# Optimization experiments

Measured on AMD Instinct MI355X. Metric: run time of the kernel, lower is better.

Reference implementation:

```python
import jax, jax.numpy as jnp
import numpy as np

GAMMA = 0.3          # surrogate gradient scale (LinearSpikeMC.gamma)
K = 2                # num_channels: multi-compartment count
T = 3                # timesteps
B = 4                # batch
LABELS = 10
CONV_CFG = [64, 64, 128, 128, 256, 256, 256, 512, 512, 512, 512, 512, 512]
POOL_AFTER = {1, 3, 6, 9}  # avg-pool after these conv indices (VGG16 'A' positions)


@jax.custom_vjp
def spike_mc(even, odd):
    # one-hot multi-compartment spike: fire where even>0 AND odd>=0
    return jnp.where((even > 0.0) & (odd >= 0.0), 1.0, 0.0).astype(even.dtype)

def _spike_fwd(even, odd):
    return spike_mc(even, odd), (even, odd)

def _spike_bwd(res, g):
    even, odd = res
    ge = GAMMA * jnp.maximum(1.0 - jnp.abs(even), 0.0) * g
    go = -GAMMA * jnp.maximum(1.0 - jnp.abs(odd), 0.0) * g
    # torch backward loop never writes the last odd compartment's grad
    go = go.at[-1].set(0.0)
    return ge, go

spike_mc.defvjp(_spike_fwd, _spike_bwd)


def conv3x3(x, w):
    return jax.lax.conv_general_dilated(
        x, w, (1, 1), 'SAME', dimension_numbers=('NCHW', 'OIHW', 'NCHW'))


def avgpool2(x):
    b, c, h, w = x.shape
    return x.reshape(b, c, h // 2, 2, w // 2, 2).mean(axis=(3, 5))


def lif(mem, syn, thr, leak):
    # leaky integrate; compartment i fires when 2^i*thr < mem <= 2^{i+1}*thr
    mem = leak * mem + syn
    pw = (2.0 ** jnp.arange(K, dtype=mem.dtype)).reshape((K,) + (1,) * mem.ndim)
    even = mem[None] / (pw * thr) - 1.0
    odd = 1.0 - mem[None] / (2.0 * pw * thr)
    sp = spike_mc(even, odd)            # [K, ...] one-hot spikes
    val = jnp.sum(pw * sp, axis=0)      # decoded value sum_i 2^i * s_i
    mem = mem - thr * val               # soft reset (reset_to_zero=0)
    return mem, val


def setup_inputs():
    key = jax.random.key(0)
    ks = jax.random.split(key, 32)
    inp = {"x": jax.random.normal(ks[0], (B, 3, 32, 32), jnp.float32)}
    in_c = 3
    for i, out_c in enumerate(CONV_CFG):
        std = float(np.sqrt(2.0 / (9.0 * out_c)))  # kaiming init from _initialize_weights2
        inp[f"w{i}"] = jax.random.normal(ks[1 + i], (out_c, in_c, 3, 3), jnp.float32) * std
        in_c = out_c
    inp["fc0"] = jax.random.normal(ks[20], (4096, 512 * 2 * 2), jnp.float32) * 0.01
    inp["fc1"] = jax.random.normal(ks[21], (4096, 4096), jnp.float32) * 0.01
    inp["fc2"] = jax.random.normal(ks[22], (LABELS, 4096), jnp.float32) * 0.01
    inp["thr"] = jnp.ones((15,), jnp.float32)   # per-layer thresholds
    inp["leak"] = jnp.ones((15,), jnp.float32)  # per-layer leaks
    return inp


def reference(x, w0, w1, w2, w3, w4, w5, w6, w7, w8, w9, w10, w11, w12,
              fc0, fc1, fc2, thr, leak):
    conv_ws = [w0, w1, w2, w3, w4, w5, w6, w7, w8, w9, w10, w11, w12]
    b = x.shape[0]
    # membranes sized at each conv's output resolution (neuron_init)
    mems = []
    s = 32
    for i, c in enumerate(CONV_CFG):
        mems.append(jnp.zeros((b, c, s, s), x.dtype))
        if i in POOL_AFTER:
            s //= 2
    carry0 = (tuple(mems),
              jnp.zeros((b, 4096), x.dtype),
              jnp.zeros((b, 4096), x.dtype),
              jnp.zeros((b, fc2.shape[0]), x.dtype))

    def step(carry, _):
        mems_c, m0, m1, logits = carry
        out = x  # analog input each timestep (input_encoding=1)
        new = []
        for i in range(13):
            m, out = lif(mems_c[i], conv3x3(out, conv_ws[i]), thr[i], leak[i])
            new.append(m)
            if i in POOL_AFTER:
                out = avgpool2(out)
        out = out.reshape(b, -1)
        m0, out = lif(m0, out @ fc0.T, thr[13], leak[13])
        m1, out = lif(m1, out @ fc1.T, thr[14], leak[14])
        logits = logits + out @ fc2.T  # final linear accumulates, no spiking
        return (tuple(new), m0, m1, logits), None

    carry, _ = jax.lax.scan(step, carry0, None, length=T)
    return carry[3]
```

## Files before the change

kernel.cpp:

```cpp
#include <hip/hip_runtime.h>


#define BATCH 4

__device__ __forceinline__ float lif_update(float mem_in, float syn, float thr,
                                            float leak, float* mem_out) {
    float m = leak * mem_in + syn;
    float val = 0.f;
    if ((m / thr - 1.f > 0.f) && (1.f - m / (2.f * thr) >= 0.f)) val += 1.f;
    if ((m / (2.f * thr) - 1.f > 0.f) && (1.f - m / (4.f * thr) >= 0.f)) val += 2.f;
    *mem_out = m - thr * val;
    return val;
}

__global__ void conv_lif0_kernel(const float* __restrict__ in,
                                 const float* __restrict__ w,
                                 float* __restrict__ out0,
                                 float* __restrict__ out1,
                                 float* __restrict__ out2,
                                 const float* __restrict__ thr_v,
                                 const float* __restrict__ leak_v,
                                 int IC, int OC, int H, int W, int n) {
    int idx = blockIdx.x * blockDim.x + threadIdx.x;
    if (idx >= n) return;
    int x  = idx % W;
    int y  = (idx / W) % H;
    int oc = (idx / (W * H)) % OC;
    int b  = idx / (W * H * OC);

    const float* wp = w + (size_t)oc * IC * 9;
    const float* ip = in + (size_t)b * IC * H * W;

    float syn = 0.f;
    for (int ic = 0; ic < IC; ++ic) {
        const float* ipc = ip + (size_t)ic * H * W;
        const float* wpc = wp + ic * 9;
#pragma unroll
        for (int ky = 0; ky < 3; ++ky) {
            int yy = y + ky - 1;
            if (yy < 0 || yy >= H) continue;
#pragma unroll
            for (int kx = 0; kx < 3; ++kx) {
                int xx = x + kx - 1;
                if (xx < 0 || xx >= W) continue;
                syn = fmaf(ipc[yy * W + xx], wpc[ky * 3 + kx], syn);
            }
        }
    }
    float thr = thr_v[0], leak = leak_v[0];
    float m = 0.f;
    float v0 = lif_update(m, syn, thr, leak, &m);
    float v1 = lif_update(m, syn, thr, leak, &m);
    float v2 = lif_update(m, syn, thr, leak, &m);
    out0[idx] = v0;
    out1[idx] = v1;
    out2[idx] = v2;
}

template <int NW, int W_>
__device__ __forceinline__ void stage_tiles(float* __restrict__ dst, int tid,
                                            int rnd, int icpw, int y0,
                                            const float* __restrict__ i0,
                                            const float* __restrict__ i1,
                                            const float* __restrict__ i2) {
    constexpr int TWD = W_ + 2;
    constexpr int TH = 64 / W_ + 2;
    constexpr int TILE = TH * TWD;
    constexpr int HW = W_ * W_;
    constexpr int TOT = NW * 3 * TILE;
    for (int s = tid; s < TOT; s += NW * 64) {
        int icg = s / (3 * TILE);
        int rem = s - icg * 3 * TILE;
        int t = rem / TILE;
        int p = rem - t * TILE;
        int r = p / TWD;
        int c = p - r * TWD;
        int ic = icg * icpw + rnd;
        int gy = y0 + r - 1;
        int gx = c - 1;
        const float* pt = (t == 0) ? i0 : ((t == 1) ? i1 : i2);
        float val = 0.f;
        if (gy >= 0 && gy < W_ && gx >= 0 && gx < W_)
            val = pt[(size_t)ic * HW + gy * W_ + gx];
        dst[s] = val;
    }
}

template <int OCT, int NW, int POOL, int W_>
__global__ __launch_bounds__(NW * 64)
void conv_mid3_kernel(const float* __restrict__ in0,
                      const float* __restrict__ in1,
                      const float* __restrict__ in2,
                      const float* __restrict__ w,
                      float* __restrict__ out0,
                      float* __restrict__ out1,
                      float* __restrict__ out2,
                      const float* __restrict__ thr_v,
                      const float* __restrict__ leak_v,
                      int layer, int IC, int OC) {
    constexpr int HW = W_ * W_;
    constexpr int RPW = 64 / W_;
    constexpr int TH = RPW + 2;
    constexpr int TWD = W_ + 2;
    constexpr int TILE = TH * TWD;
    constexpr int CHUNKS = HW / 64;

    int tid = threadIdx.x;
    int lane = tid & 63;
    int wv = tid >> 6;
    int ocg = OC / OCT;
    int bid = blockIdx.x;
    int g  = bid % ocg;
    int ch = (bid / ocg) % CHUNKS;
    int b  = bid / (ocg * CHUNKS);
    int y0 = ch * RPW;
    int oc0 = g * OCT;

    size_t boff = (size_t)b * IC * HW;
    const float* i0 = in0 + boff;
    const float* i1 = in1 + boff;
    const float* i2 = in2 + boff;
    float* const outs[3] = {out0, out1, out2};
    const float* wbase = w + (size_t)oc0 * IC * 9;

    int icpw = IC / NW;

    __shared__ float stage[2][NW * 3 * TILE];

    float acc[3][OCT];
#pragma unroll
    for (int t = 0; t < 3; ++t)
#pragma unroll
        for (int q = 0; q < OCT; ++q) acc[t][q] = 0.f;

    int r0 = lane / W_;
    int c0 = lane % W_;

    stage_tiles<NW, W_>(stage[0], tid, 0, icpw, y0, i0, i1, i2);
    __syncthreads();

    for (int rnd = 0; rnd < icpw; ++rnd) {
        int buf = rnd & 1;
        if (rnd + 1 < icpw)
            stage_tiles<NW, W_>(stage[buf ^ 1], tid, rnd + 1, icpw, y0, i0, i1, i2);

        int ic = wv * icpw + rnd;
        const float* wp = wbase + (size_t)ic * 9;
        float wvv[OCT][9];
#pragma unroll
        for (int q = 0; q < OCT; ++q) {
            const float* wq = wp + (size_t)q * IC * 9;
#pragma unroll
            for (int k = 0; k < 9; ++k) wvv[q][k] = wq[k];
        }

        const float* sb = stage[buf] + wv * (3 * TILE);
#pragma unroll
        for (int t = 0; t < 3; ++t) {
            const float* tp = sb + t * TILE + r0 * TWD + c0;
            float tv[9];
#pragma unroll
            for (int ky = 0; ky < 3; ++ky)
#pragma unroll
                for (int kx = 0; kx < 3; ++kx)
                    tv[ky * 3 + kx] = tp[ky * TWD + kx];
#pragma unroll
            for (int q = 0; q < OCT; ++q)
#pragma unroll
                for (int k = 0; k < 9; ++k)
                    acc[t][q] = fmaf(tv[k], wvv[q][k], acc[t][q]);
        }
        __syncthreads();
    }

    __shared__ float red[NW][OCT][64];
    __shared__ float vals[OCT][64];
    float thr = thr_v[layer], leak = leak_v[layer];
    float mem_reg = 0.f;
    int eq = tid >> 6, ep = tid & 63;
    constexpr int Wo = W_ / 2, Ho = W_ / 2;

#pragma unroll
    for (int t = 0; t < 3; ++t) {
        __syncthreads();
#pragma unroll
        for (int q = 0; q < OCT; ++q) red[wv][q][lane] = acc[t][q];
        __syncthreads();
        if (tid < OCT * 64) {
            float sum = 0.f;
#pragma unroll
            for (int q = 0; q < NW; ++q) sum += red[q][eq][ep];
            float val = lif_update(mem_reg, sum, thr, leak, &mem_reg);
            if (POOL) {
                vals[eq][ep] = val;
            } else {
                size_t idx = (size_t)(b * OC + oc0 + eq) * HW + ch * 64 + ep;
                outs[t][idx] = val;
            }
        }
        if (POOL) {
            __syncthreads();
            if (tid < OCT * 16) {
                int q = tid >> 4, s = tid & 15;
                int pr = s / Wo, pc = s % Wo;
                float pv = 0.25f * (vals[q][(2 * pr) * W_ + 2 * pc] +
                                    vals[q][(2 * pr) * W_ + 2 * pc + 1] +
                                    vals[q][(2 * pr + 1) * W_ + 2 * pc] +
                                    vals[q][(2 * pr + 1) * W_ + 2 * pc + 1]);
                size_t pidx = ((size_t)(b * OC + oc0 + q) * Ho +
                               (ch * (RPW >> 1) + pr)) * Wo + pc;
                outs[t][pidx] = pv;
            }
        }
    }
}

template <int S, int NW, int POOL>
__global__ __launch_bounds__(NW * 64)
void conv_small4_3_kernel(const float* __restrict__ in0,
                          const float* __restrict__ in1,
                          const float* __restrict__ in2,
                          const float* __restrict__ w,
                          float* __restrict__ out0,
                          float* __restrict__ out1,
                          float* __restrict__ out2,
                          const float* __restrict__ thr_v,
                          const float* __restrict__ leak_v,
                          int layer, int IC, int OC) {
    constexpr int SS = S * S;
    constexpr int M = 4 * SS;
    constexpr int LOG2M = (S == 4) ? 6 : 4;
    int tid = threadIdx.x;
    int lane = tid & 63;
    int wv = tid >> 6;
    int oc = blockIdx.x;

    const float* const ins[3] = {in0, in1, in2};
    float* const outs[3] = {out0, out1, out2};
    const float* wrow = w + (size_t)oc * IC * 9;

    __shared__ float red[NW][M];
    __shared__ float pvs[M];
    float thr = thr_v[layer], leak = leak_v[layer];
    float mem_reg = 0.f;

#pragma unroll
    for (int t = 0; t < 3; ++t) {
        const float* inb = ins[t];
        float acc[M];
#pragma unroll
        for (int i = 0; i < M; ++i) acc[i] = 0.f;

        for (int ic = lane + (wv << 6); ic < IC; ic += NW * 64) {
            const float* wp = wrow + (size_t)ic * 9;
            float wvv[9];
#pragma unroll
            for (int k = 0; k < 9; ++k) wvv[k] = wp[k];
#pragma unroll
            for (int b = 0; b < 4; ++b) {
                const float4* ip = (const float4*)(inb + (size_t)(b * IC + ic) * SS);
                float pv[SS];
#pragma unroll
                for (int q = 0; q < SS / 4; ++q) {
                    float4 t4 = ip[q];
                    pv[4 * q + 0] = t4.x;
                    pv[4 * q + 1] = t4.y;
                    pv[4 * q + 2] = t4.z;
                    pv[4 * q + 3] = t4.w;
                }
#pragma unroll
                for (int y = 0; y < S; ++y)
#pragma unroll
                    for (int x = 0; x < S; ++x) {
                        float a = acc[b * SS + y * S + x];
#pragma unroll
                        for (int ky = 0; ky < 3; ++ky) {
                            int yy = y + ky - 1;
                            if (yy < 0 || yy >= S) continue;
#pragma unroll
                            for (int kx = 0; kx < 3; ++kx) {
                                int xx = x + kx - 1;
                                if (xx < 0 || xx >= S) continue;
                                a = fmaf(pv[yy * S + xx], wvv[ky * 3 + kx], a);
                            }
                        }
                        acc[b * SS + y * S + x] = a;
                    }
            }
        }

#pragma unroll
        for (int step = 0; step < LOG2M; ++step) {
            const int offx = 1 << step;
            const int half = M >> (step + 1);
            const bool hi = (lane & offx) != 0;
#pragma unroll
            for (int i = 0; i < half; ++i) {
                float sent = hi ? acc[i] : acc[i + half];
                float got = __shfl_xor(sent, offx);
                acc[i] = (hi ? acc[i + half] : acc[i]) + got;
            }
        }
        float sum = acc[0];
#pragma unroll
        for (int offx = M; offx < 64; offx <<= 1) sum += __shfl_xor(sum, offx);

        __syncthreads();
        int o = (int)(__brev((unsigned)(lane & (M - 1))) >> (32 - LOG2M));
        if (lane < M) red[wv][o] = sum;
        __syncthreads();

        if (tid < M) {
            float tot = 0.f;
#pragma unroll
            for (int q = 0; q < NW; ++q) tot += red[q][tid];
            int b = tid / SS, p = tid % SS;
            float val = lif_update(mem_reg, tot, thr, leak, &mem_reg);
            if (POOL) {
                pvs[tid] = val;
            } else {
                size_t idx = (size_t)(b * OC + oc) * SS + p;
                outs[t][idx] = val;
            }
        }
        if (POOL) {
            __syncthreads();
            constexpr int Sh = S / 2, SSh = Sh * Sh;
            if (tid < 4 * SSh) {
                int b = tid / SSh, q = tid % SSh;
                int pr = q / Sh, pc = q % Sh;
                float pv = 0.25f * (pvs[b * SS + (2 * pr) * S + 2 * pc] +
                                    pvs[b * SS + (2 * pr) * S + 2 * pc + 1] +
                                    pvs[b * SS + (2 * pr + 1) * S + 2 * pc] +
                                    pvs[b * SS + (2 * pr + 1) * S + 2 * pc + 1]);
                outs[t][((size_t)(b * OC + oc) * Sh + pr) * Sh + pc] = pv;
            }
        }
    }
}

__global__ void fc_lif3_kernel(const float* __restrict__ in0,
                               const float* __restrict__ in1,
                               const float* __restrict__ in2,
                               const float* __restrict__ w,
                               float* __restrict__ out0,
                               float* __restrict__ out1,
                               float* __restrict__ out2,
                               const float* __restrict__ thr_v,
                               const float* __restrict__ leak_v,
                               int layer, int Kd, int N) {
    int wave = (blockIdx.x * blockDim.x + threadIdx.x) >> 6;
    int lane = threadIdx.x & 63;
    if (wave >= N) return;
    int j = wave;
    int K4 = Kd >> 2;
    const float4* wp = (const float4*)(w + (size_t)j * Kd);
    const float4* ip[3] = {(const float4*)in0, (const float4*)in1, (const float4*)in2};
    float* const outs[3] = {out0, out1, out2};

    float a[3][4];
#pragma unroll
    for (int t = 0; t < 3; ++t)
#pragma unroll
        for (int b = 0; b < 4; ++b) a[t][b] = 0.f;

    for (int k = lane; k < K4; k += 64) {
        float4 wv = wp[k];
#pragma unroll
        for (int t = 0; t < 3; ++t)
#pragma unroll
            for (int b = 0; b < 4; ++b) {
                float4 v = ip[t][b * K4 + k];
                a[t][b] = fmaf(wv.x, v.x, fmaf(wv.y, v.y,
                          fmaf(wv.z, v.z, fmaf(wv.w, v.w, a[t][b]))));
            }
    }
#pragma unroll
    for (int t = 0; t < 3; ++t)
#pragma unroll
        for (int b = 0; b < 4; ++b)
#pragma unroll
            for (int off = 32; off > 0; off >>= 1)
                a[t][b] += __shfl_xor(a[t][b], off);

    if (lane == 0) {
        float thr = thr_v[layer], leak = leak_v[layer];
#pragma unroll
        for (int b = 0; b < BATCH; ++b) {
            float m = 0.f;
#pragma unroll
            for (int t = 0; t < 3; ++t) {
                float val = lif_update(m, a[t][b], thr, leak, &m);
                outs[t][(size_t)b * N + j] = val;
            }
        }
    }
}

__global__ void fc2_acc3_kernel(const float* __restrict__ in0,
                                const float* __restrict__ in1,
                                const float* __restrict__ in2,
                                const float* __restrict__ w,
                                float* __restrict__ logits,
                                int Kd, int L) {
    int o = blockIdx.x;
    int l = o % L;
    int b = o / L;
    int K4 = Kd >> 2;
    const float4* ip[3] = {(const float4*)(in0 + (size_t)b * Kd),
                           (const float4*)(in1 + (size_t)b * Kd),
                           (const float4*)(in2 + (size_t)b * Kd)};
    const float4* wp = (const float4*)(w + (size_t)l * Kd);
    float st[3] = {0.f, 0.f, 0.f};
    for (int k = threadIdx.x; k < K4; k += 64) {
        float4 wv = wp[k];
#pragma unroll
        for (int t = 0; t < 3; ++t) {
            float4 iv = ip[t][k];
            st[t] = fmaf(iv.x, wv.x, fmaf(iv.y, wv.y,
                    fmaf(iv.z, wv.z, fmaf(iv.w, wv.w, st[t]))));
        }
    }
#pragma unroll
    for (int t = 0; t < 3; ++t)
#pragma unroll
        for (int off = 32; off > 0; off >>= 1) st[t] += __shfl_xor(st[t], off);
    if (threadIdx.x == 0) logits[o] = (st[0] + st[1]) + st[2];
}

extern "C" void kernel_launch(void* const* d_in, const int* in_sizes, int n_in,
                              void* d_out, int out_size, void* d_ws, size_t ws_size,
                              hipStream_t stream) {
    const float* x = (const float*)d_in[0];
    const float* convw[13];
    for (int i = 0; i < 13; ++i) convw[i] = (const float*)d_in[1 + i];
    const float* fc0 = (const float*)d_in[14];
    const float* fc1 = (const float*)d_in[15];
    const float* fc2 = (const float*)d_in[16];
    const float* thr = (const float*)d_in[17];
    const float* leak = (const float*)d_in[18];

    static const int IC[13] = {3, 64, 64, 128, 128, 256, 256, 256, 512, 512, 512, 512, 512};
    static const int OC[13] = {64, 64, 128, 128, 256, 256, 256, 512, 512, 512, 512, 512, 512};

    float* ws = (float*)d_ws;
    float* A[3];
    float* B[3];
    size_t off = 0;
    for (int i = 0; i < 3; ++i) { A[i] = ws + off; off += 262144; }
    for (int i = 0; i < 3; ++i) { B[i] = ws + off; off += 262144; }

    {
        int n = BATCH * 64 * 32 * 32;
        conv_lif0_kernel<<<(n + 255) / 256, 256, 0, stream>>>(
            x, convw[0], A[0], A[1], A[2], thr, leak, 3, 64, 32, 32, n);
    }

    float** src = A;
    float** dst = B;

    conv_mid3_kernel<4, 8, 1, 32><<<BATCH * 16 * (OC[1] / 4), 512, 0, stream>>>(
        src[0], src[1], src[2], convw[1], dst[0], dst[1], dst[2],
        thr, leak, 1, IC[1], OC[1]);
    { float** tmp = src; src = dst; dst = tmp; }

    conv_mid3_kernel<4, 8, 0, 16><<<BATCH * 4 * (OC[2] / 4), 512, 0, stream>>>(
        src[0], src[1], src[2], convw[2], dst[0], dst[1], dst[2],
        thr, leak, 2, IC[2], OC[2]);
    { float** tmp = src; src = dst; dst = tmp; }

    conv_mid3_kernel<4, 8, 1, 16><<<BATCH * 4 * (OC[3] / 4), 512, 0, stream>>>(
        src[0], src[1], src[2], convw[3], dst[0], dst[1], dst[2],
        thr, leak, 3, IC[3], OC[3]);
    { float** tmp = src; src = dst; dst = tmp; }

    conv_mid3_kernel<2, 8, 0, 8><<<BATCH * (OC[4] / 2), 512, 0, stream>>>(
        src[0], src[1], src[2], convw[4], dst[0], dst[1], dst[2],
        thr, leak, 4, IC[4], OC[4]);
    { float** tmp = src; src = dst; dst = tmp; }

    conv_mid3_kernel<2, 8, 0, 8><<<BATCH * (OC[5] / 2), 512, 0, stream>>>(
        src[0], src[1], src[2], convw[5], dst[0], dst[1], dst[2],
        thr, leak, 5, IC[5], OC[5]);
    { float** tmp = src; src = dst; dst = tmp; }

    conv_mid3_kernel<2, 8, 1, 8><<<BATCH * (OC[6] / 2), 512, 0, stream>>>(
        src[0], src[1], src[2], convw[6], dst[0], dst[1], dst[2],
        thr, leak, 6, IC[6], OC[6]);
    { float** tmp = src; src = dst; dst = tmp; }

    for (int i = 7; i <= 12; ++i) {
        if (i == 7)
            conv_small4_3_kernel<4, 4, 0><<<OC[i], 256, 0, stream>>>(
                src[0], src[1], src[2], convw[i], dst[0], dst[1], dst[2],
                thr, leak, i, IC[i], OC[i]);
        else if (i == 8)
            conv_small4_3_kernel<4, 8, 0><<<OC[i], 512, 0, stream>>>(
                src[0], src[1], src[2], convw[i], dst[0], dst[1], dst[2],
                thr, leak, i, IC[i], OC[i]);
        else if (i == 9)
            conv_small4_3_kernel<4, 8, 1><<<OC[i], 512, 0, stream>>>(
                src[0], src[1], src[2], convw[i], dst[0], dst[1], dst[2],
                thr, leak, i, IC[i], OC[i]);
        else
            conv_small4_3_kernel<2, 8, 0><<<OC[i], 512, 0, stream>>>(
                src[0], src[1], src[2], convw[i], dst[0], dst[1], dst[2],
                thr, leak, i, IC[i], OC[i]);
        float** tmp = src; src = dst; dst = tmp;
    }

    fc_lif3_kernel<<<(4096 * 64) / 256, 256, 0, stream>>>(
        src[0], src[1], src[2], fc0, dst[0], dst[1], dst[2],
        thr, leak, 13, 2048, 4096);
    { float** tmp = src; src = dst; dst = tmp; }

    fc_lif3_kernel<<<(4096 * 64) / 256, 256, 0, stream>>>(
        src[0], src[1], src[2], fc1, dst[0], dst[1], dst[2],
        thr, leak, 14, 4096, 4096);
    { float** tmp = src; src = dst; dst = tmp; }

    fc2_acc3_kernel<<<BATCH * 10, 64, 0, stream>>>(
        src[0], src[1], src[2], fc2, (float*)d_out, 4096, 10);
}
```

Before: 773.3 us.

## Stage conv weights in LDS and load inputs directly with register double-buffering

Drops the shared-memory input tile staging in the mid conv layers. Each thread now reads its 3x3 neighbourhood for all three timesteps straight from global memory with precomputed offsets and masks, keeping two channels in flight in registers. The block's full weight slice is copied into LDS once, and layer 1 moves to 8 output channels per block. This removes per-channel block barriers and global weight reloads, but relies on cache hits for the overlapping input reads and uses more LDS and registers.

```diff
diff --git a/kernel.cpp b/kernel.cpp
--- a/kernel.cpp
+++ b/kernel.cpp
@@ -57,36 +57,39 @@
     out2[idx] = v2;
 }
 
-template <int NW, int W_>
-__device__ __forceinline__ void stage_tiles(float* __restrict__ dst, int tid,
-                                            int rnd, int icpw, int y0,
-                                            const float* __restrict__ i0,
-                                            const float* __restrict__ i1,
-                                            const float* __restrict__ i2) {
-    constexpr int TWD = W_ + 2;
-    constexpr int TH = 64 / W_ + 2;
-    constexpr int TILE = TH * TWD;
-    constexpr int HW = W_ * W_;
-    constexpr int TOT = NW * 3 * TILE;
-    for (int s = tid; s < TOT; s += NW * 64) {
-        int icg = s / (3 * TILE);
-        int rem = s - icg * 3 * TILE;
-        int t = rem / TILE;
-        int p = rem - t * TILE;
-        int r = p / TWD;
-        int c = p - r * TWD;
-        int ic = icg * icpw + rnd;
-        int gy = y0 + r - 1;
-        int gx = c - 1;
-        const float* pt = (t == 0) ? i0 : ((t == 1) ? i1 : i2);
-        float val = 0.f;
-        if (gy >= 0 && gy < W_ && gx >= 0 && gx < W_)
-            val = pt[(size_t)ic * HW + gy * W_ + gx];
-        dst[s] = val;
-    }
-}
-
-template <int OCT, int NW, int POOL, int W_>
+__device__ __forceinline__ void mid_load3(float v[3][9],
+                                          const float* __restrict__ p0,
+                                          const float* __restrict__ p1,
+                                          const float* __restrict__ p2,
+                                          const int off[9], const bool msk[9]) {
+#pragma unroll
+    for (int k = 0; k < 9; ++k) {
+        v[0][k] = msk[k] ? p0[off[k]] : 0.f;
+        v[1][k] = msk[k] ? p1[off[k]] : 0.f;
+        v[2][k] = msk[k] ? p2[off[k]] : 0.f;
+    }
+}
+
+template <int OCT, int ICT>
+__device__ __forceinline__ void mid_fma3(const float v[3][9],
+                                         const float* __restrict__ wlds,
+                                         int ic, float acc[3][OCT]) {
+#pragma unroll
+    for (int q = 0; q < OCT; ++q) {
+        const float* wq = wlds + ((size_t)q * ICT + ic) * 9;
+        float wr[9];
+#pragma unroll
+        for (int k = 0; k < 9; ++k) wr[k] = wq[k];
+#pragma unroll
+        for (int k = 0; k < 9; ++k) {
+            acc[0][q] = fmaf(v[0][k], wr[k], acc[0][q]);
+            acc[1][q] = fmaf(v[1][k], wr[k], acc[1][q]);
+            acc[2][q] = fmaf(v[2][k], wr[k], acc[2][q]);
+        }
+    }
+}
+
+template <int OCT, int NW, int POOL, int ICT, int W_>
 __global__ __launch_bounds__(NW * 64)
 void conv_mid3_kernel(const float* __restrict__ in0,
                       const float* __restrict__ in1,
@@ -97,13 +100,12 @@
                       float* __restrict__ out2,
                       const float* __restrict__ thr_v,
                       const float* __restrict__ leak_v,
-                      int layer, int IC, int OC) {
+                      int layer, int OC) {
     constexpr int HW = W_ * W_;
+    constexpr int CHUNKS = HW / 64;
     constexpr int RPW = 64 / W_;
-    constexpr int TH = RPW + 2;
-    constexpr int TWD = W_ + 2;
-    constexpr int TILE = TH * TWD;
-    constexpr int CHUNKS = HW / 64;
+    constexpr int ICPW = ICT / NW;
+    static_assert((ICPW & 1) == 0, "icpw must be even");
 
     int tid = threadIdx.x;
     int lane = tid & 63;
@@ -113,19 +115,34 @@
     int g  = bid % ocg;
     int ch = (bid / ocg) % CHUNKS;
     int b  = bid / (ocg * CHUNKS);
-    int y0 = ch * RPW;
+    int y = ch * RPW + lane / W_;
+    int x = lane % W_;
     int oc0 = g * OCT;
 
-    size_t boff = (size_t)b * IC * HW;
+    int off[9];
+    bool msk[9];
+#pragma unroll
+    for (int ky = 0; ky < 3; ++ky)
+#pragma unroll
+        for (int kx = 0; kx < 3; ++kx) {
+            int yy = y + ky - 1, xx = x + kx - 1;
+            bool v = (yy >= 0 && yy < W_ && xx >= 0 && xx < W_);
+            msk[ky * 3 + kx] = v;
+            off[ky * 3 + kx] = v ? yy * W_ + xx : 0;
+        }
+
+    size_t boff = (size_t)b * ICT * HW;
     const float* i0 = in0 + boff;
     const float* i1 = in1 + boff;
     const float* i2 = in2 + boff;
     float* const outs[3] = {out0, out1, out2};
-    const float* wbase = w + (size_t)oc0 * IC * 9;
-
-    int icpw = IC / NW;
-
-    __shared__ float stage[2][NW * 3 * TILE];
+
+    __shared__ float wlds[OCT * ICT * 9];
+    {
+        const float* wsrc = w + (size_t)oc0 * ICT * 9;
+        for (int s = tid; s < OCT * ICT * 9; s += NW * 64) wlds[s] = wsrc[s];
+    }
+    __syncthreads();
 
     float acc[3][OCT];
 #pragma unroll
@@ -133,44 +150,21 @@
 #pragma unroll
         for (int q = 0; q < OCT; ++q) acc[t][q] = 0.f;
 
-    int r0 = lane / W_;
-    int c0 = lane % W_;
-
-    stage_tiles<NW, W_>(stage[0], tid, 0, icpw, y0, i0, i1, i2);
-    __syncthreads();
-
-    for (int rnd = 0; rnd < icpw; ++rnd) {
-        int buf = rnd & 1;
-        if (rnd + 1 < icpw)
-            stage_tiles<NW, W_>(stage[buf ^ 1], tid, rnd + 1, icpw, y0, i0, i1, i2);
-
-        int ic = wv * icpw + rnd;
-        const float* wp = wbase + (size_t)ic * 9;
-        float wvv[OCT][9];
-#pragma unroll
-        for (int q = 0; q < OCT; ++q) {
-            const float* wq = wp + (size_t)q * IC * 9;
-#pragma unroll
-            for (int k = 0; k < 9; ++k) wvv[q][k] = wq[k];
-        }
-
-        const float* sb = stage[buf] + wv * (3 * TILE);
-#pragma unroll
-        for (int t = 0; t < 3; ++t) {
-            const float* tp = sb + t * TILE + r0 * TWD + c0;
-            float tv[9];
-#pragma unroll
-            for (int ky = 0; ky < 3; ++ky)
-#pragma unroll
-                for (int kx = 0; kx < 3; ++kx)
-                    tv[ky * 3 + kx] = tp[ky * TWD + kx];
-#pragma unroll
-            for (int q = 0; q < OCT; ++q)
-#pragma unroll
-                for (int k = 0; k < 9; ++k)
-                    acc[t][q] = fmaf(tv[k], wvv[q][k], acc[t][q]);
-        }
-        __syncthreads();
+    int ic0 = wv * ICPW;
+    int icend = ic0 + ICPW;
+
+    float va[3][9], vb[3][9];
+    mid_load3(va, i0 + (size_t)ic0 * HW, i1 + (size_t)ic0 * HW,
+              i2 + (size_t)ic0 * HW, off, msk);
+
+    for (int ic = ic0; ic < icend; ic += 2) {
+        mid_load3(vb, i0 + (size_t)(ic + 1) * HW, i1 + (size_t)(ic + 1) * HW,
+                  i2 + (size_t)(ic + 1) * HW, off, msk);
+        mid_fma3<OCT, ICT>(va, wlds, ic, acc);
+        int icn = (ic + 2 < icend) ? ic + 2 : ic;
+        mid_load3(va, i0 + (size_t)icn * HW, i1 + (size_t)icn * HW,
+                  i2 + (size_t)icn * HW, off, msk);
+        mid_fma3<OCT, ICT>(vb, wlds, ic + 1, acc);
     }
 
     __shared__ float red[NW][OCT][64];
@@ -459,34 +453,34 @@
     float** src = A;
     float** dst = B;
 
-    conv_mid3_kernel<4, 8, 1, 32><<<BATCH * 16 * (OC[1] / 4), 512, 0, stream>>>(
+    conv_mid3_kernel<8, 8, 1, 64, 32><<<BATCH * 16 * (OC[1] / 8), 512, 0, stream>>>(
         src[0], src[1], src[2], convw[1], dst[0], dst[1], dst[2],
-        thr, leak, 1, IC[1], OC[1]);
-    { float** tmp = src; src = dst; dst = tmp; }
-
-    conv_mid3_kernel<4, 8, 0, 16><<<BATCH * 4 * (OC[2] / 4), 512, 0, stream>>>(
+        thr, leak, 1, OC[1]);
+    { float** tmp = src; src = dst; dst = tmp; }
+
+    conv_mid3_kernel<4, 8, 0, 64, 16><<<BATCH * 4 * (OC[2] / 4), 512, 0, stream>>>(
         src[0], src[1], src[2], convw[2], dst[0], dst[1], dst[2],
-        thr, leak, 2, IC[2], OC[2]);
-    { float** tmp = src; src = dst; dst = tmp; }
-
-    conv_mid3_kernel<4, 8, 1, 16><<<BATCH * 4 * (OC[3] / 4), 512, 0, stream>>>(
+        thr, leak, 2, OC[2]);
+    { float** tmp = src; src = dst; dst = tmp; }
+
+    conv_mid3_kernel<4, 8, 1, 128, 16><<<BATCH * 4 * (OC[3] / 4), 512, 0, stream>>>(
         src[0], src[1], src[2], convw[3], dst[0], dst[1], dst[2],
-        thr, leak, 3, IC[3], OC[3]);
-    { float** tmp = src; src = dst; dst = tmp; }
-
-    conv_mid3_kernel<2, 8, 0, 8><<<BATCH * (OC[4] / 2), 512, 0, stream>>>(
+        thr, leak, 3, OC[3]);
+    { float** tmp = src; src = dst; dst = tmp; }
+
+    conv_mid3_kernel<2, 8, 0, 128, 8><<<BATCH * (OC[4] / 2), 512, 0, stream>>>(
         src[0], src[1], src[2], convw[4], dst[0], dst[1], dst[2],
-        thr, leak, 4, IC[4], OC[4]);
-    { float** tmp = src; src = dst; dst = tmp; }
-
-    conv_mid3_kernel<2, 8, 0, 8><<<BATCH * (OC[5] / 2), 512, 0, stream>>>(
+        thr, leak, 4, OC[4]);
+    { float** tmp = src; src = dst; dst = tmp; }
+
+    conv_mid3_kernel<2, 8, 0, 256, 8><<<BATCH * (OC[5] / 2), 512, 0, stream>>>(
         src[0], src[1], src[2], convw[5], dst[0], dst[1], dst[2],
-        thr, leak, 5, IC[5], OC[5]);
-    { float** tmp = src; src = dst; dst = tmp; }
-
-    conv_mid3_kernel<2, 8, 1, 8><<<BATCH * (OC[6] / 2), 512, 0, stream>>>(
+        thr, leak, 5, OC[5]);
+    { float** tmp = src; src = dst; dst = tmp; }
+
+    conv_mid3_kernel<2, 8, 1, 256, 8><<<BATCH * (OC[6] / 2), 512, 0, stream>>>(
         src[0], src[1], src[2], convw[6], dst[0], dst[1], dst[2],
-        thr, leak, 6, IC[6], OC[6]);
+        thr, leak, 6, OC[6]);
     { float** tmp = src; src = dst; dst = tmp; }
 
     for (int i = 7; i <= 12; ++i) {
```

Result: faster. 692.2 us (-10.5%).
